# Performance work log

Hardware: AMD Instinct MI355X
Metric: run time of the kernel (lower is better)

## Reference

```python
import jax, jax.numpy as jnp
import numpy as np
from jax import lax


def haar_dwt2(x):
    """Level-1 Haar (db1) 2D DWT on [N, H, W] with even H, W.
    Returns cA, cH, cV (cD is discarded by the module), each [N, H//2, W//2].
    Matches pywt/ptwt db1 block form: cA=(a+b+c+d)/2, etc."""
    a = x[:, 0::2, 0::2]
    b = x[:, 0::2, 1::2]
    c = x[:, 1::2, 0::2]
    d = x[:, 1::2, 1::2]
    cA = (a + b + c + d) * 0.5
    cH = (a + b - c - d) * 0.5  # horizontal detail (highpass along rows axis)
    cV = (a - b + c - d) * 0.5  # vertical detail (highpass along cols axis)
    return cA, cH, cV


def conv2d_same(x, w, b):
    # x: [N, Cin, H, W], w: [Cout, Cin, kh, kw]
    y = lax.conv_general_dilated(x, w, window_strides=(1, 1), padding='SAME',
                                 dimension_numbers=('NCHW', 'OIHW', 'NCHW'))
    return y + b[None, :, None, None]


def maxpool2(x):
    return lax.reduce_window(x, -jnp.inf, lax.max,
                             window_dimensions=(1, 1, 2, 2),
                             window_strides=(1, 1, 2, 2), padding='VALID')


def setup_inputs() -> dict:
    key = jax.random.key(0)
    ks = jax.random.split(key, 7)
    B, C, H, W = 32, 3, 512, 512
    x = jax.random.normal(ks[0], (B, C, H, W), dtype=jnp.float32)
    # conv stack params (Conv2d(1,16,3), Conv2d(16,8,3), Conv2d(8,4,1))
    w1 = jax.random.normal(ks[1], (16, 1, 3, 3), dtype=jnp.float32) * (1.0 / 3.0)
    b1 = jnp.zeros((16,), dtype=jnp.float32)
    w2 = jax.random.normal(ks[2], (8, 16, 3, 3), dtype=jnp.float32) * (1.0 / 12.0)
    b2 = jnp.zeros((8,), dtype=jnp.float32)
    w3 = jax.random.normal(ks[3], (4, 8, 1, 1), dtype=jnp.float32) * (1.0 / 2.83)
    b3 = jnp.zeros((4,), dtype=jnp.float32)
    return {"x": x, "w1": w1, "b1": b1, "w2": w2, "b2": b2, "w3": w3, "b3": b3}


def reference(x, w1, b1, w2, b2, w3, b3):
    B, C, H, W = x.shape
    # Batch the per-image/per-channel loop: treat each channel as one map.
    flat = x.reshape(B * C, H, W)
    cA, cH, cV = haar_dwt2(flat)  # [B*C, H/2, W/2]

    # Low-frequency conv stack on approx coeffs (1 input channel per map).
    h = cA[:, None, :, :]                       # [B*C, 1, H/2, W/2]
    h = maxpool2(jax.nn.relu(conv2d_same(h, w1, b1)))
    h = maxpool2(jax.nn.relu(conv2d_same(h, w2, b2)))
    h = conv2d_same(h, w3, b3)                  # [B*C, 4, H/8, W/8]
    # per-channel flatten, then concat over channels (dim=1 in the original)
    low = h.reshape(B, 1, -1)                   # [B, 1, C*4*(H/8)*(W/8)]

    # High-frequency: per channel concat [cH.flatten(), cV.flatten()],
    # then concat over channels.
    n = (H // 2) * (W // 2)
    high = jnp.concatenate([cH.reshape(B, C, n), cV.reshape(B, C, n)], axis=-1)
    high = high.reshape(B, 1, C * 2 * n)        # [B, 1, C*2*(H/2)*(W/2)]
    return low, high
```

## Files before the change

kernel.cpp:

```cpp
#include <hip/hip_runtime.h>


typedef float v2f __attribute__((ext_vector_type(2)));

#define PK_FMA_W0(acc, w, d) \
    asm("v_pk_fma_f32 %0, %1, %2, %0 op_sel:[0,0,0] op_sel_hi:[1,0,1]" \
        : "+v"(acc) : "s"(w), "v"(d))
#define PK_FMA_W1(acc, w, d) \
    asm("v_pk_fma_f32 %0, %1, %2, %0 op_sel:[0,1,0] op_sel_hi:[1,1,1]" \
        : "+v"(acc) : "s"(w), "v"(d))
#define PK_MUL_W0(dst, w, d) \
    asm("v_pk_mul_f32 %0, %1, %2 op_sel:[0,0] op_sel_hi:[1,0]" \
        : "=v"(dst) : "s"(w), "v"(d))
#define PK_MUL_W1(dst, w, d) \
    asm("v_pk_mul_f32 %0, %1, %2 op_sel:[0,1] op_sel_hi:[1,1]" \
        : "=v"(dst) : "s"(w), "v"(d))

__global__ __launch_bounds__(256, 6) void fused_all_kernel(
    const float* __restrict__ x,
    const float* __restrict__ w1, const float* __restrict__ b1,
    const float* __restrict__ w2, const float* __restrict__ b2,
    const float* __restrict__ w3, const float* __restrict__ b3,
    float* __restrict__ outLow, float* __restrict__ outHigh)
{
    __shared__ __align__(16) float ca[38 * 70];
    __shared__ __align__(16) float h1s[4 * 18 * 34];

    int wvi = threadIdx.x >> 6;
    int lni = threadIdx.x & 63;

    int pos = threadIdx.x & 127;
    int ocg = __builtin_amdgcn_readfirstlane(threadIdx.x >> 7);
    int ly = pos >> 4, lx = pos & 15;

    #pragma unroll 1
    for (int j2 = 0; j2 < 2; ++j2) {
        int tIdx = blockIdx.x * 2 + j2;
        int img  = tIdx >> 5;
        int t    = tIdx & 31;
        int tyy = t >> 2, txx = t & 3;
        int hy0 = tyy * 16 - 1, hx0 = txx * 32 - 1;
        int cy0 = tyy * 32 - 3, cx0 = txx * 64 - 3;

        const float* xi = x + img * 262144;
        float* hb = outHigh + img * 131072;

        #pragma unroll
        for (int k = 0; k < 2; ++k) {
            int i = threadIdx.x + k * 256;
            int row = i >> 4, cg = i & 15;
            int gy = tyy * 32 + row;
            int gx = txx * 64 + cg * 4;
            const float* r0 = xi + (2 * gy) * 512 + 2 * gx;
            const float* r1 = r0 + 512;
            float4 t0 = *(const float4*)(r0);
            float4 t1 = *(const float4*)(r0 + 4);
            float4 u0 = *(const float4*)(r1);
            float4 u1 = *(const float4*)(r1 + 4);
            float4 vA, vH, vV;
            vA.x = (t0.x + t0.y + u0.x + u0.y) * 0.5f;
            vH.x = (t0.x + t0.y - u0.x - u0.y) * 0.5f;
            vV.x = (t0.x - t0.y + u0.x - u0.y) * 0.5f;
            vA.y = (t0.z + t0.w + u0.z + u0.w) * 0.5f;
            vH.y = (t0.z + t0.w - u0.z - u0.w) * 0.5f;
            vV.y = (t0.z - t0.w + u0.z - u0.w) * 0.5f;
            vA.z = (t1.x + t1.y + u1.x + u1.y) * 0.5f;
            vH.z = (t1.x + t1.y - u1.x - u1.y) * 0.5f;
            vV.z = (t1.x - t1.y + u1.x - u1.y) * 0.5f;
            vA.w = (t1.z + t1.w + u1.z + u1.w) * 0.5f;
            vH.w = (t1.z + t1.w - u1.z - u1.w) * 0.5f;
            vV.w = (t1.z - t1.w + u1.z - u1.w) * 0.5f;
            int po = (gy << 8) + gx;
            *(float4*)(hb + po) = vH;
            *(float4*)(hb + 65536 + po) = vV;
            float* cp = ca + (row + 3) * 70 + cg * 4 + 3;
            cp[0] = vA.x; cp[1] = vA.y; cp[2] = vA.z; cp[3] = vA.w;
        }

        #pragma unroll
        for (int j = 0; j < 3; ++j) {
            if (j < 2 || lni < 25) {
                int i = wvi * 153 + j * 64 + lni;
                int r, c;
                if (i < 210)      { r = i / 70;              c = i - r * 70; }
                else if (i < 420) { int jj = i - 210; r = 35 + jj / 70; c = jj - (jj / 70) * 70; }
                else              { int jj = i - 420; r = 3 + jj / 6; int k6 = jj - (jj / 6) * 6;
                                    c = (k6 < 3) ? k6 : (64 + k6); }
                int gy = cy0 + r, gx = cx0 + c;
                float v = 0.f;
                if ((unsigned)gy < 256u && (unsigned)gx < 256u) {
                    const float* p0 = xi + (2 * gy) * 512 + 2 * gx;
                    float2 a = *(const float2*)(p0);
                    float2 b = *(const float2*)(p0 + 512);
                    v = (a.x + a.y + b.x + b.y) * 0.5f;
                }
                ca[r * 70 + c] = v;
            }
        }

        v2f acc2[2][2][2];
        #pragma unroll
        for (int o2 = 0; o2 < 2; ++o2)
            #pragma unroll
            for (int r = 0; r < 2; ++r)
                #pragma unroll
                for (int c = 0; c < 2; ++c) acc2[o2][r][c] = (v2f){0.f, 0.f};

        __syncthreads();

        #pragma unroll 1
        for (int cc = 0; cc < 4; ++cc) {
            v2f wp1[2][9];
            #pragma unroll
            for (int o2 = 0; o2 < 2; ++o2)
                #pragma unroll
                for (int k = 0; k < 9; ++k)
                    wp1[o2][k] = (v2f){ w1[(cc * 4 + o2 * 2    ) * 9 + k],
                                        w1[(cc * 4 + o2 * 2 + 1) * 9 + k] };
            if (cc) __syncthreads();

            #pragma unroll 1
            for (int j = 0; j < 3; ++j) {
                if (j < 2 || lni < 25) {
                    int i = wvi * 153 + j * 64 + lni;
                    int hy = i / 34, hx = i - hy * 34;
                    const float* pb = ca + (2 * hy) * 70 + 2 * hx;
                    v2f pr[4][2];
                    #pragma unroll
                    for (int r = 0; r < 4; ++r) {
                        pr[r][0] = *(const v2f*)(pb + r * 70);
                        pr[r][1] = *(const v2f*)(pb + r * 70 + 2);
                    }
                    bool oob = ((unsigned)(hy0 + hy) >= 128u) | ((unsigned)(hx0 + hx) >= 128u);
                    v2f am[2][4];
                    #pragma unroll
                    for (int ky = 0; ky < 3; ++ky)
                    #pragma unroll
                    for (int kx = 0; kx < 3; ++kx) {
                        #pragma unroll
                        for (int o2 = 0; o2 < 2; ++o2)
                        #pragma unroll
                        for (int dy = 0; dy < 2; ++dy)
                        #pragma unroll
                        for (int dx = 0; dx < 2; ++dx) {
                            v2f d = pr[ky + dy][(kx + dx) >> 1];
                            if (ky == 0 && kx == 0) {
                                if (((kx + dx) & 1) == 0) PK_MUL_W0(am[o2][dy * 2 + dx], wp1[o2][0], d);
                                else                      PK_MUL_W1(am[o2][dy * 2 + dx], wp1[o2][0], d);
                            } else {
                                if (((kx + dx) & 1) == 0) PK_FMA_W0(am[o2][dy * 2 + dx], wp1[o2][ky * 3 + kx], d);
                                else                      PK_FMA_W1(am[o2][dy * 2 + dx], wp1[o2][ky * 3 + kx], d);
                            }
                        }
                    }
                    #pragma unroll
                    for (int o2 = 0; o2 < 2; ++o2) {
                        float mx = fmaxf(fmaxf(am[o2][0].x, am[o2][1].x),
                                         fmaxf(am[o2][2].x, am[o2][3].x));
                        float my = fmaxf(fmaxf(am[o2][0].y, am[o2][1].y),
                                         fmaxf(am[o2][2].y, am[o2][3].y));
                        mx = fmaxf(mx + b1[cc * 4 + o2 * 2    ], 0.f);
                        my = fmaxf(my + b1[cc * 4 + o2 * 2 + 1], 0.f);
                        h1s[((o2 * 2    ) * 18 + hy) * 34 + hx] = oob ? 0.f : mx;
                        h1s[((o2 * 2 + 1) * 18 + hy) * 34 + hx] = oob ? 0.f : my;
                    }
                }
            }
            __syncthreads();

            #pragma unroll
            for (int icl = 0; icl < 4; ++icl) {
                int ic = cc * 4 + icl;
                v2f wl[2][9];
                #pragma unroll
                for (int o2 = 0; o2 < 2; ++o2) {
                    int oc0 = ocg * 4 + o2 * 2;
                    #pragma unroll
                    for (int k = 0; k < 9; ++k)
                        wl[o2][k] = (v2f){ w2[((oc0    ) * 16 + ic) * 9 + k],
                                           w2[((oc0 + 1) * 16 + ic) * 9 + k] };
                }
                const float* base = h1s + (icl * 18 + ly * 2) * 34 + lx * 2;
                v2f wr[4][2];
                #pragma unroll
                for (int r = 0; r < 4; ++r) {
                    wr[r][0] = *(const v2f*)(base + r * 34);
                    wr[r][1] = *(const v2f*)(base + r * 34 + 2);
                }
                #pragma unroll
                for (int ky = 0; ky < 3; ++ky)
                #pragma unroll
                for (int kx = 0; kx < 3; ++kx)
                #pragma unroll
                for (int o2 = 0; o2 < 2; ++o2) {
                    #pragma unroll
                    for (int r = 0; r < 2; ++r)
                    #pragma unroll
                    for (int c = 0; c < 2; ++c) {
                        v2f d = wr[r + ky][(c + kx) >> 1];
                        if (((c + kx) & 1) == 0) PK_FMA_W0(acc2[o2][r][c], wl[o2][ky * 3 + kx], d);
                        else                     PK_FMA_W1(acc2[o2][r][c], wl[o2][ky * 3 + kx], d);
                    }
                }
            }
        }

        float h2v[4];
        #pragma unroll
        for (int o2 = 0; o2 < 2; ++o2) {
            float mx = fmaxf(fmaxf(acc2[o2][0][0].x, acc2[o2][0][1].x),
                             fmaxf(acc2[o2][1][0].x, acc2[o2][1][1].x));
            float my = fmaxf(fmaxf(acc2[o2][0][0].y, acc2[o2][0][1].y),
                             fmaxf(acc2[o2][1][0].y, acc2[o2][1][1].y));
            h2v[o2 * 2    ] = fmaxf(mx + b2[ocg * 4 + o2 * 2    ], 0.f);
            h2v[o2 * 2 + 1] = fmaxf(my + b2[ocg * 4 + o2 * 2 + 1], 0.f);
        }
        __syncthreads();
        float* hx2 = h1s;
        #pragma unroll
        for (int j = 0; j < 4; ++j) hx2[pos * 9 + ocg * 4 + j] = h2v[j];
        __syncthreads();

        float hv[8];
        #pragma unroll
        for (int ic = 0; ic < 8; ++ic) hv[ic] = hx2[pos * 9 + ic];
        float* dst = outLow + img * 16384;
        int posg = (tyy * 8 + ly) * 64 + txx * 16 + lx;
        #pragma unroll
        for (int jo = 0; jo < 2; ++jo) {
            int oc3 = ocg * 2 + jo;
            float s = b3[oc3];
            #pragma unroll
            for (int ic = 0; ic < 8; ++ic) s += w3[oc3 * 8 + ic] * hv[ic];
            dst[oc3 * 4096 + posg] = s;
        }
    }
}

extern "C" void kernel_launch(void* const* d_in, const int* in_sizes, int n_in,
                              void* d_out, int out_size, void* d_ws, size_t ws_size,
                              hipStream_t stream) {
    const float* x  = (const float*)d_in[0];
    const float* w1 = (const float*)d_in[1];
    const float* b1 = (const float*)d_in[2];
    const float* w2 = (const float*)d_in[3];
    const float* b2 = (const float*)d_in[4];
    const float* w3 = (const float*)d_in[5];
    const float* b3 = (const float*)d_in[6];
    float* out     = (float*)d_out;
    float* outLow  = out;
    float* outHigh = out + 1572864;

    fused_all_kernel<<<1536, 256, 0, stream>>>(x, w1, b1, w2, b2, w3, b3,
                                               outLow, outHigh);
}
```

Before: 226.8 us.

## Rebalance tile work across 2048 blocks with full and half-height tiles

Each block now processes one full 32x64 tile plus one half-height 16x64 tile instead of two full tiles. The grid goes from 1536 to 2048 blocks and launch bounds are raised to 8 waves per SIMD. The aim is better load balance and occupancy across the CUs, avoiding a partial last wave of blocks. The cost is a larger halo-to-interior ratio on the half tiles, which means extra redundant halo loads and compute, plus possible register spills under the tighter launch bound.

```diff
diff --git a/kernel.cpp b/kernel.cpp
--- a/kernel.cpp
+++ b/kernel.cpp
@@ -16,7 +16,7 @@
     asm("v_pk_mul_f32 %0, %1, %2 op_sel:[0,1] op_sel_hi:[1,1]" \
         : "=v"(dst) : "s"(w), "v"(d))
 
-__global__ __launch_bounds__(256, 6) void fused_all_kernel(
+__global__ __launch_bounds__(256, 8) void fused_all_kernel(
     const float* __restrict__ x,
     const float* __restrict__ w1, const float* __restrict__ b1,
     const float* __restrict__ w2, const float* __restrict__ b2,
@@ -26,16 +26,10 @@
     __shared__ __align__(16) float ca[38 * 70];
     __shared__ __align__(16) float h1s[4 * 18 * 34];
 
-    int wvi = threadIdx.x >> 6;
-    int lni = threadIdx.x & 63;
-
-    int pos = threadIdx.x & 127;
-    int ocg = __builtin_amdgcn_readfirstlane(threadIdx.x >> 7);
-    int ly = pos >> 4, lx = pos & 15;
-
-    #pragma unroll 1
-    for (int j2 = 0; j2 < 2; ++j2) {
-        int tIdx = blockIdx.x * 2 + j2;
+    int tid = threadIdx.x;
+
+    {
+        int tIdx = blockIdx.x;
         int img  = tIdx >> 5;
         int t    = tIdx & 31;
         int tyy = t >> 2, txx = t & 3;
@@ -47,7 +41,7 @@
 
         #pragma unroll
         for (int k = 0; k < 2; ++k) {
-            int i = threadIdx.x + k * 256;
+            int i = tid + k * 256;
             int row = i >> 4, cg = i & 15;
             int gy = tyy * 32 + row;
             int gx = txx * 64 + cg * 4;
@@ -77,26 +71,27 @@
             cp[0] = vA.x; cp[1] = vA.y; cp[2] = vA.z; cp[3] = vA.w;
         }
 
-        #pragma unroll
-        for (int j = 0; j < 3; ++j) {
-            if (j < 2 || lni < 25) {
-                int i = wvi * 153 + j * 64 + lni;
-                int r, c;
-                if (i < 210)      { r = i / 70;              c = i - r * 70; }
-                else if (i < 420) { int jj = i - 210; r = 35 + jj / 70; c = jj - (jj / 70) * 70; }
-                else              { int jj = i - 420; r = 3 + jj / 6; int k6 = jj - (jj / 6) * 6;
-                                    c = (k6 < 3) ? k6 : (64 + k6); }
-                int gy = cy0 + r, gx = cx0 + c;
-                float v = 0.f;
-                if ((unsigned)gy < 256u && (unsigned)gx < 256u) {
-                    const float* p0 = xi + (2 * gy) * 512 + 2 * gx;
-                    float2 a = *(const float2*)(p0);
-                    float2 b = *(const float2*)(p0 + 512);
-                    v = (a.x + a.y + b.x + b.y) * 0.5f;
-                }
-                ca[r * 70 + c] = v;
-            }
-        }
+        #pragma unroll 1
+        for (int i = tid; i < 612; i += 256) {
+            int r, c;
+            if (i < 210)      { r = i / 70;              c = i - r * 70; }
+            else if (i < 420) { int j = i - 210; r = 35 + j / 70; c = j - (j / 70) * 70; }
+            else              { int j = i - 420; r = 3 + j / 6; int k6 = j - (j / 6) * 6;
+                                c = (k6 < 3) ? k6 : (64 + k6); }
+            int gy = cy0 + r, gx = cx0 + c;
+            float v = 0.f;
+            if ((unsigned)gy < 256u && (unsigned)gx < 256u) {
+                const float* p0 = xi + (2 * gy) * 512 + 2 * gx;
+                float2 a = *(const float2*)(p0);
+                float2 b = *(const float2*)(p0 + 512);
+                v = (a.x + a.y + b.x + b.y) * 0.5f;
+            }
+            ca[r * 70 + c] = v;
+        }
+
+        int pos = tid & 127;
+        int ocg = __builtin_amdgcn_readfirstlane(tid >> 7);
+        int ly = pos >> 4, lx = pos & 15;
 
         v2f acc2[2][2][2];
         #pragma unroll
@@ -120,50 +115,47 @@
             if (cc) __syncthreads();
 
             #pragma unroll 1
-            for (int j = 0; j < 3; ++j) {
-                if (j < 2 || lni < 25) {
-                    int i = wvi * 153 + j * 64 + lni;
-                    int hy = i / 34, hx = i - hy * 34;
-                    const float* pb = ca + (2 * hy) * 70 + 2 * hx;
-                    v2f pr[4][2];
-                    #pragma unroll
-                    for (int r = 0; r < 4; ++r) {
-                        pr[r][0] = *(const v2f*)(pb + r * 70);
-                        pr[r][1] = *(const v2f*)(pb + r * 70 + 2);
-                    }
-                    bool oob = ((unsigned)(hy0 + hy) >= 128u) | ((unsigned)(hx0 + hx) >= 128u);
-                    v2f am[2][4];
-                    #pragma unroll
-                    for (int ky = 0; ky < 3; ++ky)
-                    #pragma unroll
-                    for (int kx = 0; kx < 3; ++kx) {
-                        #pragma unroll
-                        for (int o2 = 0; o2 < 2; ++o2)
-                        #pragma unroll
-                        for (int dy = 0; dy < 2; ++dy)
-                        #pragma unroll
-                        for (int dx = 0; dx < 2; ++dx) {
-                            v2f d = pr[ky + dy][(kx + dx) >> 1];
-                            if (ky == 0 && kx == 0) {
-                                if (((kx + dx) & 1) == 0) PK_MUL_W0(am[o2][dy * 2 + dx], wp1[o2][0], d);
-                                else                      PK_MUL_W1(am[o2][dy * 2 + dx], wp1[o2][0], d);
-                            } else {
-                                if (((kx + dx) & 1) == 0) PK_FMA_W0(am[o2][dy * 2 + dx], wp1[o2][ky * 3 + kx], d);
-                                else                      PK_FMA_W1(am[o2][dy * 2 + dx], wp1[o2][ky * 3 + kx], d);
-                            }
+            for (int i = tid; i < 612; i += 256) {
+                int hy = i / 34, hx = i - hy * 34;
+                const float* pb = ca + (2 * hy) * 70 + 2 * hx;
+                v2f pr[4][2];
+                #pragma unroll
+                for (int r = 0; r < 4; ++r) {
+                    pr[r][0] = *(const v2f*)(pb + r * 70);
+                    pr[r][1] = *(const v2f*)(pb + r * 70 + 2);
+                }
+                bool oob = ((unsigned)(hy0 + hy) >= 128u) | ((unsigned)(hx0 + hx) >= 128u);
+                v2f am[2][4];
+                #pragma unroll
+                for (int ky = 0; ky < 3; ++ky)
+                #pragma unroll
+                for (int kx = 0; kx < 3; ++kx) {
+                    #pragma unroll
+                    for (int o2 = 0; o2 < 2; ++o2)
+                    #pragma unroll
+                    for (int dy = 0; dy < 2; ++dy)
+                    #pragma unroll
+                    for (int dx = 0; dx < 2; ++dx) {
+                        v2f d = pr[ky + dy][(kx + dx) >> 1];
+                        if (ky == 0 && kx == 0) {
+                            if (((kx + dx) & 1) == 0) PK_MUL_W0(am[o2][dy * 2 + dx], wp1[o2][0], d);
+                            else                      PK_MUL_W1(am[o2][dy * 2 + dx], wp1[o2][0], d);
+                        } else {
+                            if (((kx + dx) & 1) == 0) PK_FMA_W0(am[o2][dy * 2 + dx], wp1[o2][ky * 3 + kx], d);
+                            else                      PK_FMA_W1(am[o2][dy * 2 + dx], wp1[o2][ky * 3 + kx], d);
                         }
                     }
-                    #pragma unroll
-                    for (int o2 = 0; o2 < 2; ++o2) {
-                        float mx = fmaxf(fmaxf(am[o2][0].x, am[o2][1].x),
-                                         fmaxf(am[o2][2].x, am[o2][3].x));
-                        float my = fmaxf(fmaxf(am[o2][0].y, am[o2][1].y),
-                                         fmaxf(am[o2][2].y, am[o2][3].y));
-                        mx = fmaxf(mx + b1[cc * 4 + o2 * 2    ], 0.f);
-                        my = fmaxf(my + b1[cc * 4 + o2 * 2 + 1], 0.f);
-                        h1s[((o2 * 2    ) * 18 + hy) * 34 + hx] = oob ? 0.f : mx;
-                        h1s[((o2 * 2 + 1) * 18 + hy) * 34 + hx] = oob ? 0.f : my;
-                    }
+                }
+                #pragma unroll
+                for (int o2 = 0; o2 < 2; ++o2) {
+                    float mx = fmaxf(fmaxf(am[o2][0].x, am[o2][1].x),
+                                     fmaxf(am[o2][2].x, am[o2][3].x));
+                    float my = fmaxf(fmaxf(am[o2][0].y, am[o2][1].y),
+                                     fmaxf(am[o2][2].y, am[o2][3].y));
+                    mx = fmaxf(mx + b1[cc * 4 + o2 * 2    ], 0.f);
+                    my = fmaxf(my + b1[cc * 4 + o2 * 2 + 1], 0.f);
+                    h1s[((o2 * 2    ) * 18 + hy) * 34 + hx] = oob ? 0.f : mx;
+                    h1s[((o2 * 2 + 1) * 18 + hy) * 34 + hx] = oob ? 0.f : my;
                 }
             }
             __syncthreads();
@@ -234,6 +226,198 @@
             for (int ic = 0; ic < 8; ++ic) s += w3[oc3 * 8 + ic] * hv[ic];
             dst[oc3 * 4096 + posg] = s;
         }
+    }
+
+    {
+        int b  = blockIdx.x;
+        int t2 = 2048 + (b >> 1);
+        int img = t2 >> 5;
+        int t   = t2 & 31;
+        int rs = ((t >> 2) << 1) + (b & 1);
+        int cs = t & 3;
+        int hy0 = rs * 8 - 1, hx0 = cs * 32 - 1;
+        int cy0 = rs * 16 - 3, cx0 = cs * 64 - 3;
+
+        const float* xi = x + img * 262144;
+        float* hb = outHigh + img * 131072;
+
+        {
+            int i = tid;
+            int row = i >> 4, cg = i & 15;
+            int gy = rs * 16 + row;
+            int gx = cs * 64 + cg * 4;
+            const float* r0 = xi + (2 * gy) * 512 + 2 * gx;
+            const float* r1 = r0 + 512;
+            float4 t0 = *(const float4*)(r0);
+            float4 t1 = *(const float4*)(r0 + 4);
+            float4 u0 = *(const float4*)(r1);
+            float4 u1 = *(const float4*)(r1 + 4);
+            float4 vA, vH, vV;
+            vA.x = (t0.x + t0.y + u0.x + u0.y) * 0.5f;
+            vH.x = (t0.x + t0.y - u0.x - u0.y) * 0.5f;
+            vV.x = (t0.x - t0.y + u0.x - u0.y) * 0.5f;
+            vA.y = (t0.z + t0.w + u0.z + u0.w) * 0.5f;
+            vH.y = (t0.z + t0.w - u0.z - u0.w) * 0.5f;
+            vV.y = (t0.z - t0.w + u0.z - u0.w) * 0.5f;
+            vA.z = (t1.x + t1.y + u1.x + u1.y) * 0.5f;
+            vH.z = (t1.x + t1.y - u1.x - u1.y) * 0.5f;
+            vV.z = (t1.x - t1.y + u1.x - u1.y) * 0.5f;
+            vA.w = (t1.z + t1.w + u1.z + u1.w) * 0.5f;
+            vH.w = (t1.z + t1.w - u1.z - u1.w) * 0.5f;
+            vV.w = (t1.z - t1.w + u1.z - u1.w) * 0.5f;
+            int po = (gy << 8) + gx;
+            *(float4*)(hb + po) = vH;
+            *(float4*)(hb + 65536 + po) = vV;
+            float* cp = ca + (row + 3) * 70 + cg * 4 + 3;
+            cp[0] = vA.x; cp[1] = vA.y; cp[2] = vA.z; cp[3] = vA.w;
+        }
+
+        #pragma unroll 1
+        for (int i = tid; i < 516; i += 256) {
+            int r, c;
+            if (i < 210)      { r = i / 70;              c = i - r * 70; }
+            else if (i < 420) { int j = i - 210; r = 19 + j / 70; c = j - (j / 70) * 70; }
+            else              { int j = i - 420; r = 3 + j / 6; int k6 = j - (j / 6) * 6;
+                                c = (k6 < 3) ? k6 : (64 + k6); }
+            int gy = cy0 + r, gx = cx0 + c;
+            float v = 0.f;
+            if ((unsigned)gy < 256u && (unsigned)gx < 256u) {
+                const float* p0 = xi + (2 * gy) * 512 + 2 * gx;
+                float2 a = *(const float2*)(p0);
+                float2 b2v = *(const float2*)(p0 + 512);
+                v = (a.x + a.y + b2v.x + b2v.y) * 0.5f;
+            }
+            ca[r * 70 + c] = v;
+        }
+
+        int pos = tid & 63;
+        int ocg = __builtin_amdgcn_readfirstlane(tid >> 6);
+        int ly = pos >> 4, lx = pos & 15;
+
+        v2f acc2[2][2];
+        #pragma unroll
+        for (int r = 0; r < 2; ++r)
+            #pragma unroll
+            for (int c = 0; c < 2; ++c) acc2[r][c] = (v2f){0.f, 0.f};
+
+        __syncthreads();
+
+        #pragma unroll 1
+        for (int cc = 0; cc < 4; ++cc) {
+            v2f wp1[2][9];
+            #pragma unroll
+            for (int o2 = 0; o2 < 2; ++o2)
+                #pragma unroll
+                for (int k = 0; k < 9; ++k)
+                    wp1[o2][k] = (v2f){ w1[(cc * 4 + o2 * 2    ) * 9 + k],
+                                        w1[(cc * 4 + o2 * 2 + 1) * 9 + k] };
+            if (cc) __syncthreads();
+
+            #pragma unroll 1
+            for (int i = tid; i < 340; i += 256) {
+                int hy = i / 34, hx = i - hy * 34;
+                const float* pb = ca + (2 * hy) * 70 + 2 * hx;
+                v2f pr[4][2];
+                #pragma unroll
+                for (int r = 0; r < 4; ++r) {
+                    pr[r][0] = *(const v2f*)(pb + r * 70);
+                    pr[r][1] = *(const v2f*)(pb + r * 70 + 2);
+                }
+                bool oob = ((unsigned)(hy0 + hy) >= 128u) | ((unsigned)(hx0 + hx) >= 128u);
+                v2f am[2][4];
+                #pragma unroll
+                for (int ky = 0; ky < 3; ++ky)
+                #pragma unroll
+                for (int kx = 0; kx < 3; ++kx) {
+                    #pragma unroll
+                    for (int o2 = 0; o2 < 2; ++o2)
+                    #pragma unroll
+                    for (int dy = 0; dy < 2; ++dy)
+                    #pragma unroll
+                    for (int dx = 0; dx < 2; ++dx) {
+                        v2f d = pr[ky + dy][(kx + dx) >> 1];
+                        if (ky == 0 && kx == 0) {
+                            if (((kx + dx) & 1) == 0) PK_MUL_W0(am[o2][dy * 2 + dx], wp1[o2][0], d);
+                            else                      PK_MUL_W1(am[o2][dy * 2 + dx], wp1[o2][0], d);
+                        } else {
+                            if (((kx + dx) & 1) == 0) PK_FMA_W0(am[o2][dy * 2 + dx], wp1[o2][ky * 3 + kx], d);
+                            else                      PK_FMA_W1(am[o2][dy * 2 + dx], wp1[o2][ky * 3 + kx], d);
+                        }
+                    }
+                }
+                #pragma unroll
+                for (int o2 = 0; o2 < 2; ++o2) {
+                    float mx = fmaxf(fmaxf(am[o2][0].x, am[o2][1].x),
+                                     fmaxf(am[o2][2].x, am[o2][3].x));
+                    float my = fmaxf(fmaxf(am[o2][0].y, am[o2][1].y),
+                                     fmaxf(am[o2][2].y, am[o2][3].y));
+                    mx = fmaxf(mx + b1[cc * 4 + o2 * 2    ], 0.f);
+                    my = fmaxf(my + b1[cc * 4 + o2 * 2 + 1], 0.f);
+                    h1s[((o2 * 2    ) * 10 + hy) * 34 + hx] = oob ? 0.f : mx;
+                    h1s[((o2 * 2 + 1) * 10 + hy) * 34 + hx] = oob ? 0.f : my;
+                }
+            }
+            __syncthreads();
+
+            #pragma unroll
+            for (int icl = 0; icl < 4; ++icl) {
+                int ic = cc * 4 + icl;
+                v2f wl[9];
+                {
+                    int oc0 = ocg * 2;
+                    #pragma unroll
+                    for (int k = 0; k < 9; ++k)
+                        wl[k] = (v2f){ w2[((oc0    ) * 16 + ic) * 9 + k],
+                                       w2[((oc0 + 1) * 16 + ic) * 9 + k] };
+                }
+                const float* base = h1s + (icl * 10 + ly * 2) * 34 + lx * 2;
+                v2f wr[4][2];
+                #pragma unroll
+                for (int r = 0; r < 4; ++r) {
+                    wr[r][0] = *(const v2f*)(base + r * 34);
+                    wr[r][1] = *(const v2f*)(base + r * 34 + 2);
+                }
+                #pragma unroll
+                for (int ky = 0; ky < 3; ++ky)
+                #pragma unroll
+                for (int kx = 0; kx < 3; ++kx) {
+                    #pragma unroll
+                    for (int r = 0; r < 2; ++r)
+                    #pragma unroll
+                    for (int c = 0; c < 2; ++c) {
+                        v2f d = wr[r + ky][(c + kx) >> 1];
+                        if (((c + kx) & 1) == 0) PK_FMA_W0(acc2[r][c], wl[ky * 3 + kx], d);
+                        else                     PK_FMA_W1(acc2[r][c], wl[ky * 3 + kx], d);
+                    }
+                }
+            }
+        }
+
+        float h2a, h2b;
+        {
+            float mx = fmaxf(fmaxf(acc2[0][0].x, acc2[0][1].x),
+                             fmaxf(acc2[1][0].x, acc2[1][1].x));
+            float my = fmaxf(fmaxf(acc2[0][0].y, acc2[0][1].y),
+                             fmaxf(acc2[1][0].y, acc2[1][1].y));
+            h2a = fmaxf(mx + b2[ocg * 2    ], 0.f);
+            h2b = fmaxf(my + b2[ocg * 2 + 1], 0.f);
+        }
+        __syncthreads();
+        float* hx2 = h1s;
+        hx2[pos * 9 + ocg * 2    ] = h2a;
+        hx2[pos * 9 + ocg * 2 + 1] = h2b;
+        __syncthreads();
+
+        float hv[8];
+        #pragma unroll
+        for (int ic = 0; ic < 8; ++ic) hv[ic] = hx2[pos * 9 + ic];
+        float* dst = outLow + img * 16384;
+        int posg = (rs * 4 + ly) * 64 + cs * 16 + lx;
+        int oc3 = ocg;
+        float sacc = b3[oc3];
+        #pragma unroll
+        for (int ic = 0; ic < 8; ++ic) sacc += w3[oc3 * 8 + ic] * hv[ic];
+        dst[oc3 * 4096 + posg] = sacc;
     }
 }
 
@@ -251,6 +435,6 @@
     float* outLow  = out;
     float* outHigh = out + 1572864;
 
-    fused_all_kernel<<<1536, 256, 0, stream>>>(x, w1, b1, w2, b2, w3, b3,
+    fused_all_kernel<<<2048, 256, 0, stream>>>(x, w1, b1, w2, b2, w3, b3,
                                                outLow, outHigh);
 }
```

Result: no change. 224.7 us (-0.9%).

## Schedule tiles dynamically via an atomic counter in a persistent-style grid

Applied to the files above, without the earlier changes.

Each block used to own two fixed tiles. Blocks now repeatedly claim the next tile index from a global atomic counter in workspace until all 3072 tiles are taken. Occupancy hint rises from 6 to 7 blocks per SIMD, and the grid becomes 1792 blocks sized to the device. Within a tile, the per-wave element split is replaced by a simple thread-strided loop. The aim is to balance load and cut tail effects, at the cost of a memset launch, an atomic plus barrier per tile, and possible register pressure from the tighter launch bound.

```diff
diff --git a/kernel.cpp b/kernel.cpp
--- a/kernel.cpp
+++ b/kernel.cpp
@@ -16,26 +16,26 @@
     asm("v_pk_mul_f32 %0, %1, %2 op_sel:[0,1] op_sel_hi:[1,1]" \
         : "=v"(dst) : "s"(w), "v"(d))
 
-__global__ __launch_bounds__(256, 6) void fused_all_kernel(
+__global__ __launch_bounds__(256, 7) void fused_all_kernel(
     const float* __restrict__ x,
     const float* __restrict__ w1, const float* __restrict__ b1,
     const float* __restrict__ w2, const float* __restrict__ b2,
     const float* __restrict__ w3, const float* __restrict__ b3,
-    float* __restrict__ outLow, float* __restrict__ outHigh)
+    float* __restrict__ outLow, float* __restrict__ outHigh,
+    unsigned int* __restrict__ counter)
 {
     __shared__ __align__(16) float ca[38 * 70];
     __shared__ __align__(16) float h1s[4 * 18 * 34];
-
-    int wvi = threadIdx.x >> 6;
-    int lni = threadIdx.x & 63;
-
-    int pos = threadIdx.x & 127;
-    int ocg = __builtin_amdgcn_readfirstlane(threadIdx.x >> 7);
-    int ly = pos >> 4, lx = pos & 15;
-
-    #pragma unroll 1
-    for (int j2 = 0; j2 < 2; ++j2) {
-        int tIdx = blockIdx.x * 2 + j2;
+    __shared__ int s_tile;
+
+    int tid = threadIdx.x;
+
+    for (;;) {
+        if (tid == 0) s_tile = (int)atomicAdd(counter, 1u);
+        __syncthreads();
+        int tIdx = s_tile;
+        if (tIdx >= 3072) break;
+
         int img  = tIdx >> 5;
         int t    = tIdx & 31;
         int tyy = t >> 2, txx = t & 3;
@@ -47,7 +47,7 @@
 
         #pragma unroll
         for (int k = 0; k < 2; ++k) {
-            int i = threadIdx.x + k * 256;
+            int i = tid + k * 256;
             int row = i >> 4, cg = i & 15;
             int gy = tyy * 32 + row;
             int gx = txx * 64 + cg * 4;
@@ -77,26 +77,27 @@
             cp[0] = vA.x; cp[1] = vA.y; cp[2] = vA.z; cp[3] = vA.w;
         }
 
-        #pragma unroll
-        for (int j = 0; j < 3; ++j) {
-            if (j < 2 || lni < 25) {
-                int i = wvi * 153 + j * 64 + lni;
-                int r, c;
-                if (i < 210)      { r = i / 70;              c = i - r * 70; }
-                else if (i < 420) { int jj = i - 210; r = 35 + jj / 70; c = jj - (jj / 70) * 70; }
-                else              { int jj = i - 420; r = 3 + jj / 6; int k6 = jj - (jj / 6) * 6;
-                                    c = (k6 < 3) ? k6 : (64 + k6); }
-                int gy = cy0 + r, gx = cx0 + c;
-                float v = 0.f;
-                if ((unsigned)gy < 256u && (unsigned)gx < 256u) {
-                    const float* p0 = xi + (2 * gy) * 512 + 2 * gx;
-                    float2 a = *(const float2*)(p0);
-                    float2 b = *(const float2*)(p0 + 512);
-                    v = (a.x + a.y + b.x + b.y) * 0.5f;
-                }
-                ca[r * 70 + c] = v;
+        #pragma unroll 1
+        for (int i = tid; i < 612; i += 256) {
+            int r, c;
+            if (i < 210)      { r = i / 70;              c = i - r * 70; }
+            else if (i < 420) { int j = i - 210; r = 35 + j / 70; c = j - (j / 70) * 70; }
+            else              { int j = i - 420; r = 3 + j / 6; int k6 = j - (j / 6) * 6;
+                                c = (k6 < 3) ? k6 : (64 + k6); }
+            int gy = cy0 + r, gx = cx0 + c;
+            float v = 0.f;
+            if ((unsigned)gy < 256u && (unsigned)gx < 256u) {
+                const float* p0 = xi + (2 * gy) * 512 + 2 * gx;
+                float2 a = *(const float2*)(p0);
+                float2 b = *(const float2*)(p0 + 512);
+                v = (a.x + a.y + b.x + b.y) * 0.5f;
             }
-        }
+            ca[r * 70 + c] = v;
+        }
+
+        int pos = tid & 127;
+        int ocg = __builtin_amdgcn_readfirstlane(tid >> 7);
+        int ly = pos >> 4, lx = pos & 15;
 
         v2f acc2[2][2][2];
         #pragma unroll
@@ -120,50 +121,47 @@
             if (cc) __syncthreads();
 
             #pragma unroll 1
-            for (int j = 0; j < 3; ++j) {
-                if (j < 2 || lni < 25) {
-                    int i = wvi * 153 + j * 64 + lni;
-                    int hy = i / 34, hx = i - hy * 34;
-                    const float* pb = ca + (2 * hy) * 70 + 2 * hx;
-                    v2f pr[4][2];
-                    #pragma unroll
-                    for (int r = 0; r < 4; ++r) {
-                        pr[r][0] = *(const v2f*)(pb + r * 70);
-                        pr[r][1] = *(const v2f*)(pb + r * 70 + 2);
-                    }
-                    bool oob = ((unsigned)(hy0 + hy) >= 128u) | ((unsigned)(hx0 + hx) >= 128u);
-                    v2f am[2][4];
-                    #pragma unroll
-                    for (int ky = 0; ky < 3; ++ky)
-                    #pragma unroll
-                    for (int kx = 0; kx < 3; ++kx) {
-                        #pragma unroll
-                        for (int o2 = 0; o2 < 2; ++o2)
-                        #pragma unroll
-                        for (int dy = 0; dy < 2; ++dy)
-                        #pragma unroll
-                        for (int dx = 0; dx < 2; ++dx) {
-                            v2f d = pr[ky + dy][(kx + dx) >> 1];
-                            if (ky == 0 && kx == 0) {
-                                if (((kx + dx) & 1) == 0) PK_MUL_W0(am[o2][dy * 2 + dx], wp1[o2][0], d);
-                                else                      PK_MUL_W1(am[o2][dy * 2 + dx], wp1[o2][0], d);
-                            } else {
-                                if (((kx + dx) & 1) == 0) PK_FMA_W0(am[o2][dy * 2 + dx], wp1[o2][ky * 3 + kx], d);
-                                else                      PK_FMA_W1(am[o2][dy * 2 + dx], wp1[o2][ky * 3 + kx], d);
-                            }
+            for (int i = tid; i < 612; i += 256) {
+                int hy = i / 34, hx = i - hy * 34;
+                const float* pb = ca + (2 * hy) * 70 + 2 * hx;
+                v2f pr[4][2];
+                #pragma unroll
+                for (int r = 0; r < 4; ++r) {
+                    pr[r][0] = *(const v2f*)(pb + r * 70);
+                    pr[r][1] = *(const v2f*)(pb + r * 70 + 2);
+                }
+                bool oob = ((unsigned)(hy0 + hy) >= 128u) | ((unsigned)(hx0 + hx) >= 128u);
+                v2f am[2][4];
+                #pragma unroll
+                for (int ky = 0; ky < 3; ++ky)
+                #pragma unroll
+                for (int kx = 0; kx < 3; ++kx) {
+                    #pragma unroll
+                    for (int o2 = 0; o2 < 2; ++o2)
+                    #pragma unroll
+                    for (int dy = 0; dy < 2; ++dy)
+                    #pragma unroll
+                    for (int dx = 0; dx < 2; ++dx) {
+                        v2f d = pr[ky + dy][(kx + dx) >> 1];
+                        if (ky == 0 && kx == 0) {
+                            if (((kx + dx) & 1) == 0) PK_MUL_W0(am[o2][dy * 2 + dx], wp1[o2][0], d);
+                            else                      PK_MUL_W1(am[o2][dy * 2 + dx], wp1[o2][0], d);
+                        } else {
+                            if (((kx + dx) & 1) == 0) PK_FMA_W0(am[o2][dy * 2 + dx], wp1[o2][ky * 3 + kx], d);
+                            else                      PK_FMA_W1(am[o2][dy * 2 + dx], wp1[o2][ky * 3 + kx], d);
                         }
                     }
-                    #pragma unroll
-                    for (int o2 = 0; o2 < 2; ++o2) {
-                        float mx = fmaxf(fmaxf(am[o2][0].x, am[o2][1].x),
-                                         fmaxf(am[o2][2].x, am[o2][3].x));
-                        float my = fmaxf(fmaxf(am[o2][0].y, am[o2][1].y),
-                                         fmaxf(am[o2][2].y, am[o2][3].y));
-                        mx = fmaxf(mx + b1[cc * 4 + o2 * 2    ], 0.f);
-                        my = fmaxf(my + b1[cc * 4 + o2 * 2 + 1], 0.f);
-                        h1s[((o2 * 2    ) * 18 + hy) * 34 + hx] = oob ? 0.f : mx;
-                        h1s[((o2 * 2 + 1) * 18 + hy) * 34 + hx] = oob ? 0.f : my;
-                    }
+                }
+                #pragma unroll
+                for (int o2 = 0; o2 < 2; ++o2) {
+                    float mx = fmaxf(fmaxf(am[o2][0].x, am[o2][1].x),
+                                     fmaxf(am[o2][2].x, am[o2][3].x));
+                    float my = fmaxf(fmaxf(am[o2][0].y, am[o2][1].y),
+                                     fmaxf(am[o2][2].y, am[o2][3].y));
+                    mx = fmaxf(mx + b1[cc * 4 + o2 * 2    ], 0.f);
+                    my = fmaxf(my + b1[cc * 4 + o2 * 2 + 1], 0.f);
+                    h1s[((o2 * 2    ) * 18 + hy) * 34 + hx] = oob ? 0.f : mx;
+                    h1s[((o2 * 2 + 1) * 18 + hy) * 34 + hx] = oob ? 0.f : my;
                 }
             }
             __syncthreads();
@@ -250,7 +248,9 @@
     float* out     = (float*)d_out;
     float* outLow  = out;
     float* outHigh = out + 1572864;
-
-    fused_all_kernel<<<1536, 256, 0, stream>>>(x, w1, b1, w2, b2, w3, b3,
-                                               outLow, outHigh);
+    unsigned int* counter = (unsigned int*)d_ws;
+
+    hipMemsetAsync(counter, 0, sizeof(unsigned int), stream);
+    fused_all_kernel<<<1792, 256, 0, stream>>>(x, w1, b1, w2, b2, w3, b3,
+                                               outLow, outHigh, counter);
 }
```

Measured after the change: 231.5 us. 2.1% more time.
